# Kernel optimization log

Measured on AMD Instinct MI355X. Metric: run time of the kernel, lower is better.

Reference implementation:

```python
import jax, jax.numpy as jnp
import numpy as np

B, K, N, M = 32, 128, 128, 256  # batch, num_classes(==n_dim), n_dim, samples-per-matrix
EPSILON = 0.1
LAMBDA_SOFTMAX = 0.1
LEARNING_RATE = 0.01
BN_EPS = 1e-5


def setup_inputs() -> dict:
    key = jax.random.key(0)
    k1, k2, k3 = jax.random.split(key, 3)
    x = jax.random.normal(k1, (B, N, M), dtype=jnp.float32)
    A = jax.random.normal(k2, (K, N, N), dtype=jnp.float32) * 0.1
    EC_proto = jnp.einsum('kij,klj->kil', A, A)  # per-class PSD prototype covariances (K,N,N)
    EC_count = jax.random.uniform(k3, (K,), dtype=jnp.float32, minval=1.0, maxval=100.0)
    return {"x": x, "EC_proto": EC_proto, "EC_count": EC_count}


def reference(x, EC_proto, EC_count):
    n = x.shape[1]
    dtype = x.dtype
    # BatchNorm1d(num_classes, affine=False, track_running_stats=False): batch stats over (N, L)
    mean = x.mean(axis=(0, 2), keepdims=True)
    var = x.var(axis=(0, 2), keepdims=True)  # biased variance, as torch uses for normalization
    x = (x - mean) / jnp.sqrt(var + BN_EPS)

    eye = jnp.eye(n, dtype=dtype)
    total = EC_count.sum()
    has_counts = total > 1e-6

    # E branch: global expansion operator
    e_alpha = jnp.where(has_counts, n / (EPSILON * EPSILON * total), jnp.zeros((), dtype))
    e = e_alpha * jnp.linalg.inv(e_alpha * EC_proto.sum(0) + eye)  # (N,N)
    e_x_z = jnp.einsum('ij,bjm->bim', e, x)  # (B,N,M)

    # C branch: per-class compression operators
    bool_depth = (EC_count != 0).astype(dtype)  # (K,)
    count_fix = EC_count + (1.0 - bool_depth)
    c_alpha = (n / (count_fix * EPSILON * EPSILON) * bool_depth)[:, None, None]  # (K,1,1)
    c = c_alpha * jnp.linalg.inv(c_alpha * EC_proto + eye[None])  # (K,N,N)
    c_x_z = jnp.einsum('kij,bjm->bkim', c, x)  # (B,K,N,M)

    # Frobenius norm per (b,k), rescaled to sum to 10 over classes
    norm = jnp.sqrt((c_x_z * c_x_z).sum(axis=(2, 3)))  # (B,K)
    norm = 10.0 * norm / norm.sum(axis=1, keepdims=True)

    pi = jax.nn.softmax(-LAMBDA_SOFTMAX * norm, axis=1) * bool_depth  # (B,K)
    gama = jnp.where(has_counts, EC_count / total, jnp.zeros_like(EC_count))  # (K,)

    z_d = e_x_z - jnp.einsum('k,bkim,bk->bim', gama, c_x_z, pi)  # (B,N,M)
    return x + LEARNING_RATE * z_d
```

## Files before the change

### kernel.cpp

```cpp
#include <hip/hip_runtime.h>
#include <math.h>

#define Bb 32
#define Kk 128
#define Nn 128
#define Mm 256
#define EPS2 0.01f
#define LAMBDA_S 0.1f
#define LR 0.01f
#define BN_EPS_C 1e-5f

#define SWZ(c) (((c) & 14) | (((c) & 1) << 4) | (((c) >> 4) & 1))

__global__ void kA_bn_psum(const float* __restrict__ x, const float* __restrict__ P,
                           float* __restrict__ xn, float* __restrict__ Psum) {
  int t = threadIdx.x;
  if (blockIdx.x < 128) {
    int n = blockIdx.x;
    float s = 0.f, s2 = 0.f;
    #pragma unroll 4
    for (int b = 0; b < Bb; ++b) {
      float v = x[(size_t)b * (Nn * Mm) + n * Mm + t];
      s += v;
      s2 += v * v;
    }
    #pragma unroll
    for (int o = 32; o > 0; o >>= 1) {
      s += __shfl_down(s, o, 64);
      s2 += __shfl_down(s2, o, 64);
    }
    __shared__ float rs[4], rs2[4];
    if ((t & 63) == 0) { rs[t >> 6] = s; rs2[t >> 6] = s2; }
    __syncthreads();
    float S = rs[0] + rs[1] + rs[2] + rs[3];
    float S2 = rs2[0] + rs2[1] + rs2[2] + rs2[3];
    float mean = S * (1.0f / (Bb * Mm));
    float var = S2 * (1.0f / (Bb * Mm)) - mean * mean;
    float rstd = 1.0f / sqrtf(var + BN_EPS_C);
    #pragma unroll 4
    for (int b = 0; b < Bb; ++b) {
      size_t idx = (size_t)b * (Nn * Mm) + n * Mm + t;
      xn[idx] = (x[idx] - mean) * rstd;
    }
  } else {
    int e = (blockIdx.x - 128) * 256 + t;
    float s = 0.f;
    #pragma unroll 8
    for (int k = 0; k < Kk; ++k) s += P[(size_t)k * 16384 + e];
    Psum[e] = s;
  }
}

__global__ __launch_bounds__(256, 1) void k3S(
    const float* __restrict__ P, const float* __restrict__ Psum,
    const float* __restrict__ cnt, float* __restrict__ C,
    const float* __restrict__ xn, float* __restrict__ S) {
  __shared__ __align__(16) float LB[8448];
  int bx = blockIdx.x;
  int t = threadIdx.x;

  if (bx < 129) {
    float* Mt = LB;
    float* Rb = LB + 2112;
    float* redc = LB + 4160;
    int blk = bx;
    int tx = t & 15, ty = t >> 4;

    float cv = cnt[t & 127];
    float sr = cv;
    #pragma unroll
    for (int o = 32; o > 0; o >>= 1) sr += __shfl_down(sr, o, 64);
    if ((t & 63) == 0) redc[t >> 6] = sr;
    __syncthreads();
    float total = redc[0] + redc[1];
    bool has = total > 1e-6f;
    float av;
    if (blk < 128) {
      float c = cnt[blk];
      float bk = (c != 0.0f) ? 1.0f : 0.0f;
      float cfix = c + (1.0f - bk);
      av = (float)Nn / (cfix * EPS2) * bk;
    } else {
      av = has ? ((float)Nn / (EPS2 * total)) : 0.0f;
    }
    const float* src = (blk < 128) ? (P + (size_t)blk * 16384) : Psum;

    float a[8][8];
    #pragma unroll
    for (int i = 0; i < 8; ++i) {
      int row = ty * 8 + i;
      float4 p0 = *(const float4*)&src[row * 128 + tx * 8];
      float4 p1 = *(const float4*)&src[row * 128 + tx * 8 + 4];
      a[i][0] = av * p0.x; a[i][1] = av * p0.y; a[i][2] = av * p0.z; a[i][3] = av * p0.w;
      a[i][4] = av * p1.x; a[i][5] = av * p1.y; a[i][6] = av * p1.z; a[i][7] = av * p1.w;
      if (tx == ty) a[i][i] += 1.0f;
    }

    for (int kb = 0; kb < 8; ++kb) {
      int k0 = kb * 16;
      if ((ty >> 1) == kb) {
        int d = ty & 1;
        #pragma unroll
        for (int i = 0; i < 8; ++i) {
          *(float4*)&Rb[(d * 8 + i) * 128 + SWZ(2 * tx) * 4] =
              make_float4(a[i][0], a[i][1], a[i][2], a[i][3]);
          *(float4*)&Rb[(d * 8 + i) * 128 + SWZ(2 * tx + 1) * 4] =
              make_float4(a[i][4], a[i][5], a[i][6], a[i][7]);
        }
      }
      if ((tx >> 1) == kb) {
        int dh = tx & 1;
        #pragma unroll
        for (int i = 0; i < 8; ++i)
          #pragma unroll
          for (int j = 0; j < 8; ++j)
            Mt[(dh * 8 + j) * 132 + ty * 8 + i] = a[i][j];
      }
      __syncthreads();

      if (t < 64) {
        int l = t;
        float m[2][16];
        #pragma unroll
        for (int d = 0; d < 2; ++d)
          #pragma unroll
          for (int j = 0; j < 16; ++j)
            m[d][j] = Mt[j * 132 + 2 * l + d];
        #pragma unroll
        for (int q = 0; q < 16; ++q) {
          int lq = (k0 + q) >> 1;
          float pr[16];
          #pragma unroll
          for (int j = 0; j < 16; ++j) pr[j] = __shfl(m[q & 1][j], lq, 64);
          float pinv = 1.0f / pr[q];
          #pragma unroll
          for (int d = 0; d < 2; ++d) {
            float f = m[d][q];
            bool isp = (2 * l + d == k0 + q);
            float g = isp ? (1.0f - pinv) : f * pinv;
            #pragma unroll
            for (int j = 0; j < 16; ++j) m[d][j] = fmaf(-g, pr[j], m[d][j]);
            m[d][q] = isp ? pinv : -g;
          }
        }
        #pragma unroll
        for (int d = 0; d < 2; ++d)
          #pragma unroll
          for (int j = 0; j < 16; ++j)
            Mt[j * 132 + 2 * l + d] = m[d][j];
      }
      __syncthreads();

      if ((ty >> 1) == kb) {
        #pragma unroll
        for (int i = 0; i < 8; ++i)
          #pragma unroll
          for (int j = 0; j < 8; ++j) a[i][j] = 0.0f;
      }
      #pragma unroll
      for (int q = 0; q < 16; ++q) {
        float4 m0 = *(const float4*)&Mt[q * 132 + ty * 8];
        float4 m1 = *(const float4*)&Mt[q * 132 + ty * 8 + 4];
        float4 r0 = *(const float4*)&Rb[q * 128 + SWZ(2 * tx) * 4];
        float4 r1 = *(const float4*)&Rb[q * 128 + SWZ(2 * tx + 1) * 4];
        float mq[8] = {m0.x, m0.y, m0.z, m0.w, m1.x, m1.y, m1.z, m1.w};
        float rq[8] = {r0.x, r0.y, r0.z, r0.w, r1.x, r1.y, r1.z, r1.w};
        #pragma unroll
        for (int i = 0; i < 8; ++i)
          #pragma unroll
          for (int j = 0; j < 8; ++j)
            a[i][j] = fmaf(mq[i], rq[j], a[i][j]);
      }
      if ((tx >> 1) == kb) {
        int dh = tx & 1;
        #pragma unroll
        for (int j = 0; j < 8; ++j) {
          float4 v0 = *(const float4*)&Mt[(dh * 8 + j) * 132 + ty * 8];
          float4 v1 = *(const float4*)&Mt[(dh * 8 + j) * 132 + ty * 8 + 4];
          a[0][j] = v0.x; a[1][j] = v0.y; a[2][j] = v0.z; a[3][j] = v0.w;
          a[4][j] = v1.x; a[5][j] = v1.y; a[6][j] = v1.z; a[7][j] = v1.w;
        }
      }
      __syncthreads();
    }

    float* dst = C + (size_t)blk * 16384;
    #pragma unroll
    for (int i = 0; i < 8; ++i) {
      int row = ty * 8 + i;
      float4 v0 = make_float4(av * a[i][0], av * a[i][1], av * a[i][2], av * a[i][3]);
      float4 v1 = make_float4(av * a[i][4], av * a[i][5], av * a[i][6], av * a[i][7]);
      *(float4*)&dst[row * 128 + tx * 8] = v0;
      *(float4*)&dst[row * 128 + tx * 8 + 4] = v1;
    }
  } else {
    int bxx = bx - 129;
    int b = bxx >> 1;
    int jbase = (bxx & 1) * 64;
    float* X = LB;
    int tx = t & 15, ty = t >> 4;
    float acc[8][4] = {};
    for (int mc = 0; mc < Mm; mc += 64) {
      __syncthreads();
      for (int c = 0; c < 32; ++c) {
        int e = c * 256 + t;
        int i = e >> 6, mm = e & 63;
        X[i * 65 + mm] = xn[(size_t)b * (Nn * Mm) + i * Mm + mc + mm];
      }
      __syncthreads();
      for (int mm = 0; mm < 64; ++mm) {
        float ai[8], bj[4];
        #pragma unroll
        for (int q = 0; q < 8; ++q) ai[q] = X[(ty * 8 + q) * 65 + mm];
        #pragma unroll
        for (int q = 0; q < 4; ++q) bj[q] = X[(jbase + tx * 4 + q) * 65 + mm];
        #pragma unroll
        for (int qi = 0; qi < 8; ++qi)
          #pragma unroll
          for (int qj = 0; qj < 4; ++qj)
            acc[qi][qj] = fmaf(ai[qi], bj[qj], acc[qi][qj]);
      }
    }
    float* dst = S + (size_t)b * 16384;
    #pragma unroll
    for (int qi = 0; qi < 8; ++qi) {
      float4 v = make_float4(acc[qi][0], acc[qi][1], acc[qi][2], acc[qi][3]);
      *(float4*)&dst[(ty * 8 + qi) * 128 + jbase + tx * 4] = v;
    }
  }
}

__global__ __launch_bounds__(256, 1) void gram_k(const float* __restrict__ C,
                                                 float* __restrict__ G) {
  __shared__ __align__(16) float LB[128 * 128];
  int k = blockIdx.x >> 1, half = blockIdx.x & 1;
  int t = threadIdx.x;
  const float* src = C + (size_t)k * 16384;
  for (int c = 0; c < 64; ++c) LB[c * 256 + t] = src[c * 256 + t];
  __syncthreads();
  int tx = t & 31, ty = t >> 5;
  int i0 = half * 64 + ty * 8, j0 = tx * 4;
  float acc[8][4] = {};
  for (int l = 0; l < 128; ++l) {
    float ai[8], bj[4];
    *(float4*)&ai[0] = *(const float4*)&LB[l * 128 + i0];
    *(float4*)&ai[4] = *(const float4*)&LB[l * 128 + i0 + 4];
    *(float4*)&bj[0] = *(const float4*)&LB[l * 128 + j0];
    #pragma unroll
    for (int qi = 0; qi < 8; ++qi)
      #pragma unroll
      for (int qj = 0; qj < 4; ++qj)
        acc[qi][qj] = fmaf(ai[qi], bj[qj], acc[qi][qj]);
  }
  float* dst = G + (size_t)k * 16384;
  #pragma unroll
  for (int qi = 0; qi < 8; ++qi)
    *(float4*)&dst[(i0 + qi) * 128 + j0] =
        make_float4(acc[qi][0], acc[qi][1], acc[qi][2], acc[qi][3]);
}

__global__ __launch_bounds__(256, 1) void k6_k(const float* __restrict__ G,
                                               const float* __restrict__ S,
                                               float* __restrict__ part) {
  __shared__ __align__(16) float Gp[128 * 68];
  __shared__ __align__(16) float Sp[32 * 68];
  int c = blockIdx.x;
  int t = threadIdx.x;
  int off = c * 64;
  #pragma unroll
  for (int q = 0; q < 8; ++q) {
    int e = q * 256 + t;
    int k = e >> 4, j4 = e & 15;
    *(float4*)&Gp[k * 68 + j4 * 4] = *(const float4*)&G[(size_t)k * 16384 + off + j4 * 4];
  }
  #pragma unroll
  for (int q = 0; q < 2; ++q) {
    int e = q * 256 + t;
    int b = e >> 4, j4 = e & 15;
    *(float4*)&Sp[b * 68 + j4 * 4] = *(const float4*)&S[(size_t)b * 16384 + off + j4 * 4];
  }
  __syncthreads();
  int tk = t & 15, tb = t >> 4;
  float acc[2][8] = {};
  for (int j4 = 0; j4 < 16; ++j4) {
    float4 sv0 = *(const float4*)&Sp[(tb * 2) * 68 + j4 * 4];
    float4 sv1 = *(const float4*)&Sp[(tb * 2 + 1) * 68 + j4 * 4];
    float4 gv[8];
    #pragma unroll
    for (int q = 0; q < 8; ++q) gv[q] = *(const float4*)&Gp[(tk + 16 * q) * 68 + j4 * 4];
    #pragma unroll
    for (int q = 0; q < 8; ++q) {
      acc[0][q] = fmaf(sv0.x, gv[q].x, acc[0][q]);
      acc[0][q] = fmaf(sv0.y, gv[q].y, acc[0][q]);
      acc[0][q] = fmaf(sv0.z, gv[q].z, acc[0][q]);
      acc[0][q] = fmaf(sv0.w, gv[q].w, acc[0][q]);
      acc[1][q] = fmaf(sv1.x, gv[q].x, acc[1][q]);
      acc[1][q] = fmaf(sv1.y, gv[q].y, acc[1][q]);
      acc[1][q] = fmaf(sv1.z, gv[q].z, acc[1][q]);
      acc[1][q] = fmaf(sv1.w, gv[q].w, acc[1][q]);
    }
  }
  float* pout = part + (size_t)c * 4096;
  #pragma unroll
  for (int bb = 0; bb < 2; ++bb)
    #pragma unroll
    for (int q = 0; q < 8; ++q)
      pout[(tb * 2 + bb) * 128 + tk + 16 * q] = acc[bb][q];
}

__global__ void k7_k(const float* __restrict__ part,
                     const float* __restrict__ cnt, float* __restrict__ wT) {
  int b = blockIdx.x;
  int t = threadIdx.x;
  int k = t & 127, h = t >> 7;
  float s = 0.f;
  #pragma unroll 8
  for (int c = h * 128; c < h * 128 + 128; ++c)
    s += part[(size_t)c * 4096 + b * 128 + k];
  __shared__ float sh[256];
  sh[t] = s;
  __syncthreads();
  float norm2 = sh[k] + sh[k + 128];
  float norm = sqrtf(fmaxf(norm2, 0.0f));
  float cv = cnt[k];
  float tt = cv;
  #pragma unroll
  for (int o = 32; o > 0; o >>= 1) tt += __shfl_down(tt, o, 64);
  __shared__ float redt[4];
  if ((t & 63) == 0) redt[t >> 6] = tt;
  float r = norm;
  #pragma unroll
  for (int o = 32; o > 0; o >>= 1) r += __shfl_down(r, o, 64);
  __shared__ float red[4];
  if ((t & 63) == 0) red[t >> 6] = r;
  __syncthreads();
  float total = redt[0] + redt[1];
  float sumn = 0.5f * (red[0] + red[1] + red[2] + red[3]);
  float nr = 10.0f * norm / fmaxf(sumn, 1e-30f);
  float ex = expf(-LAMBDA_S * nr);
  float r2 = ex;
  #pragma unroll
  for (int o = 32; o > 0; o >>= 1) r2 += __shfl_down(r2, o, 64);
  __shared__ float red2[4];
  if ((t & 63) == 0) red2[t >> 6] = r2;
  __syncthreads();
  float sume = 0.5f * (red2[0] + red2[1] + red2[2] + red2[3]);
  float bk = (cv != 0.0f) ? 1.0f : 0.0f;
  float pi = (ex / sume) * bk;
  float gama = (total > 1e-6f) ? (cv / total) : 0.0f;
  if (h == 0) wT[k * 32 + b] = gama * pi;
}

__global__ __launch_bounds__(256, 1) void k8_k(const float* __restrict__ C,
                                               const float* __restrict__ E,
                                               const float* __restrict__ wT,
                                               float* __restrict__ F) {
  int e = blockIdx.x * 256 + threadIdx.x;
  int b0 = blockIdx.y * 8;
  float acc[8];
  float ev = E[e];
  #pragma unroll
  for (int b = 0; b < 8; ++b) acc[b] = ev;
  for (int k = 0; k < 128; ++k) {
    float cv = C[(size_t)k * 16384 + e];
    const float* wk = wT + k * 32 + b0;
    #pragma unroll
    for (int b = 0; b < 8; ++b) acc[b] = fmaf(-wk[b], cv, acc[b]);
  }
  #pragma unroll
  for (int b = 0; b < 8; ++b) F[(size_t)(b0 + b) * 16384 + e] = acc[b];
}

__global__ __launch_bounds__(256, 1) void k9_k(const float* __restrict__ F,
                                               const float* __restrict__ xn,
                                               float* __restrict__ out) {
  int bx = blockIdx.x;
  int b = bx >> 3, y = bx & 7;
  int mq = y >> 1, ih = y & 1;
  __shared__ __align__(16) float Ft[64 * 68];
  __shared__ __align__(16) float Xt[64 * 68];
  int t = threadIdx.x;
  int tx = t & 15, ty = t >> 4;
  float acc[4][4] = {};
  for (int jc = 0; jc < 128; jc += 64) {
    __syncthreads();
    #pragma unroll
    for (int q = 0; q < 4; ++q) {
      int e = q * 256 + t;
      int i = e >> 4, j4 = e & 15;
      *(float4*)&Ft[i * 68 + j4 * 4] =
          *(const float4*)&F[(size_t)b * 16384 + (ih * 64 + i) * 128 + jc + j4 * 4];
    }
    #pragma unroll
    for (int q = 0; q < 4; ++q) {
      int e = q * 256 + t;
      int jj = e >> 4, m4 = e & 15;
      *(float4*)&Xt[jj * 68 + m4 * 4] =
          *(const float4*)&xn[(size_t)b * (Nn * Mm) + (jc + jj) * Mm + mq * 64 + m4 * 4];
    }
    __syncthreads();
    for (int j4 = 0; j4 < 16; ++j4) {
      float4 fi[4], xm[4];
      #pragma unroll
      for (int r = 0; r < 4; ++r)
        fi[r] = *(const float4*)&Ft[(ty * 4 + r) * 68 + j4 * 4];
      #pragma unroll
      for (int r = 0; r < 4; ++r)
        xm[r] = *(const float4*)&Xt[(j4 * 4 + r) * 68 + tx * 4];
      #pragma unroll
      for (int qi = 0; qi < 4; ++qi) {
        #pragma unroll
        for (int qm = 0; qm < 4; ++qm) {
          float xv = ((const float*)&xm[0])[qm];
          acc[qi][qm] = fmaf(fi[qi].x, xv, acc[qi][qm]);
          xv = ((const float*)&xm[1])[qm];
          acc[qi][qm] = fmaf(fi[qi].y, xv, acc[qi][qm]);
          xv = ((const float*)&xm[2])[qm];
          acc[qi][qm] = fmaf(fi[qi].z, xv, acc[qi][qm]);
          xv = ((const float*)&xm[3])[qm];
          acc[qi][qm] = fmaf(fi[qi].w, xv, acc[qi][qm]);
        }
      }
    }
  }
  int i0 = ih * 64 + ty * 4, m0 = mq * 64 + tx * 4;
  #pragma unroll
  for (int qi = 0; qi < 4; ++qi) {
    float4 xv = *(const float4*)&xn[(size_t)b * (Nn * Mm) + (i0 + qi) * Mm + m0];
    float4 o;
    o.x = fmaf(LR, acc[qi][0], xv.x);
    o.y = fmaf(LR, acc[qi][1], xv.y);
    o.z = fmaf(LR, acc[qi][2], xv.z);
    o.w = fmaf(LR, acc[qi][3], xv.w);
    *(float4*)&out[(size_t)b * (Nn * Mm) + (i0 + qi) * Mm + m0] = o;
  }
}

extern "C" void kernel_launch(void* const* d_in, const int* in_sizes, int n_in,
                              void* d_out, int out_size, void* d_ws, size_t ws_size,
                              hipStream_t stream) {
  const float* x = (const float*)d_in[0];
  const float* P = (const float*)d_in[1];
  const float* cnt = (const float*)d_in[2];
  float* out = (float*)d_out;

  float* ws = (float*)d_ws;
  float* xn = ws;
  float* C = xn + 1048576;
  float* G = C + 2113536;
  float* S = G + 2097152;
  float* part = S + 524288;
  float* F = part + 1048576;
  float* wT = F + 524288;
  float* Psum = wT + 4096;
  size_t need_bytes = (size_t)((Psum + 16384) - ws) * sizeof(float);
  if (ws_size < need_bytes) return;

  hipLaunchKernelGGL(kA_bn_psum, dim3(192), dim3(256), 0, stream, x, P, xn, Psum);
  hipLaunchKernelGGL(k3S, dim3(193), dim3(256), 0, stream, P, Psum, cnt, C, xn, S);
  hipLaunchKernelGGL(gram_k, dim3(256), dim3(256), 0, stream, C, G);
  hipLaunchKernelGGL(k6_k, dim3(256), dim3(256), 0, stream, G, S, part);
  hipLaunchKernelGGL(k7_k, dim3(32), dim3(256), 0, stream, part, cnt, wT);
  hipLaunchKernelGGL(k8_k, dim3(64, 4), dim3(256), 0, stream, C,
                     C + (size_t)128 * 16384, wT, F);
  hipLaunchKernelGGL(k9_k, dim3(256), dim3(256), 0, stream, F, xn, out);
}
```

Before: 177.5 us.

## Fuse Gram-norm contraction and softmax-weighted apply into two kernels

Merges the Gram computation with the per-batch norm contraction so the Gram matrices stay in shared memory and are reduced directly against S, never written to global memory. Also merges the softmax weighting, the weighted sum of compression operators and the final apply GEMM into one kernel that keeps F in shared memory. This cuts five launches to two and removes the large global round-trips for G, part and F. The cost is that the softmax is recomputed serially by eight threads per block, and the apply kernel has only 128 blocks and reads xn straight from global memory without tiling, which may leave the GPU underused.

```diff
diff --git a/kernel.cpp b/kernel.cpp
--- a/kernel.cpp
+++ b/kernel.cpp
@@ -230,16 +230,18 @@
   }
 }
 
-__global__ __launch_bounds__(256, 1) void gram_k(const float* __restrict__ C,
-                                                 float* __restrict__ G) {
+__global__ __launch_bounds__(256, 1) void kGN(const float* __restrict__ C,
+                                              const float* __restrict__ S,
+                                              float* __restrict__ norm2h) {
   __shared__ __align__(16) float LB[128 * 128];
-  int k = blockIdx.x >> 1, half = blockIdx.x & 1;
+  __shared__ float redb[4][32];
+  int k = blockIdx.x >> 1, h = blockIdx.x & 1;
   int t = threadIdx.x;
   const float* src = C + (size_t)k * 16384;
   for (int c = 0; c < 64; ++c) LB[c * 256 + t] = src[c * 256 + t];
   __syncthreads();
-  int tx = t & 31, ty = t >> 5;
-  int i0 = half * 64 + ty * 8, j0 = tx * 4;
+  int tx = t & 15, ty = t >> 4;
+  int i0 = ty * 8, j0 = h * 64 + tx * 4;
   float acc[8][4] = {};
   for (int l = 0; l < 128; ++l) {
     float ai[8], bj[4];
@@ -252,187 +254,159 @@
       for (int qj = 0; qj < 4; ++qj)
         acc[qi][qj] = fmaf(ai[qi], bj[qj], acc[qi][qj]);
   }
-  float* dst = G + (size_t)k * 16384;
+  __syncthreads();
   #pragma unroll
   for (int qi = 0; qi < 8; ++qi)
-    *(float4*)&dst[(i0 + qi) * 128 + j0] =
+    *(float4*)&LB[(i0 + qi) * 64 + tx * 4] =
         make_float4(acc[qi][0], acc[qi][1], acc[qi][2], acc[qi][3]);
-}
-
-__global__ __launch_bounds__(256, 1) void k6_k(const float* __restrict__ G,
-                                               const float* __restrict__ S,
-                                               float* __restrict__ part) {
-  __shared__ __align__(16) float Gp[128 * 68];
-  __shared__ __align__(16) float Sp[32 * 68];
-  int c = blockIdx.x;
-  int t = threadIdx.x;
-  int off = c * 64;
+  __syncthreads();
+  float nacc[32];
+  #pragma unroll
+  for (int b = 0; b < 32; ++b) nacc[b] = 0.0f;
   #pragma unroll
   for (int q = 0; q < 8; ++q) {
-    int e = q * 256 + t;
-    int k = e >> 4, j4 = e & 15;
-    *(float4*)&Gp[k * 68 + j4 * 4] = *(const float4*)&G[(size_t)k * 16384 + off + j4 * 4];
+    int el = (q * 256 + t) * 4;
+    float4 g = *(const float4*)&LB[el];
+    int i = el >> 6, jl = el & 63;
+    const float* sb = S + i * 128 + h * 64 + jl;
+    #pragma unroll
+    for (int b = 0; b < 32; ++b) {
+      float4 sv = *(const float4*)&sb[(size_t)b * 16384];
+      nacc[b] = fmaf(g.x, sv.x, nacc[b]);
+      nacc[b] = fmaf(g.y, sv.y, nacc[b]);
+      nacc[b] = fmaf(g.z, sv.z, nacc[b]);
+      nacc[b] = fmaf(g.w, sv.w, nacc[b]);
+    }
   }
   #pragma unroll
-  for (int q = 0; q < 2; ++q) {
-    int e = q * 256 + t;
-    int b = e >> 4, j4 = e & 15;
-    *(float4*)&Sp[b * 68 + j4 * 4] = *(const float4*)&S[(size_t)b * 16384 + off + j4 * 4];
-  }
-  __syncthreads();
-  int tk = t & 15, tb = t >> 4;
-  float acc[2][8] = {};
-  for (int j4 = 0; j4 < 16; ++j4) {
-    float4 sv0 = *(const float4*)&Sp[(tb * 2) * 68 + j4 * 4];
-    float4 sv1 = *(const float4*)&Sp[(tb * 2 + 1) * 68 + j4 * 4];
-    float4 gv[8];
-    #pragma unroll
-    for (int q = 0; q < 8; ++q) gv[q] = *(const float4*)&Gp[(tk + 16 * q) * 68 + j4 * 4];
-    #pragma unroll
-    for (int q = 0; q < 8; ++q) {
-      acc[0][q] = fmaf(sv0.x, gv[q].x, acc[0][q]);
-      acc[0][q] = fmaf(sv0.y, gv[q].y, acc[0][q]);
-      acc[0][q] = fmaf(sv0.z, gv[q].z, acc[0][q]);
-      acc[0][q] = fmaf(sv0.w, gv[q].w, acc[0][q]);
-      acc[1][q] = fmaf(sv1.x, gv[q].x, acc[1][q]);
-      acc[1][q] = fmaf(sv1.y, gv[q].y, acc[1][q]);
-      acc[1][q] = fmaf(sv1.z, gv[q].z, acc[1][q]);
-      acc[1][q] = fmaf(sv1.w, gv[q].w, acc[1][q]);
-    }
-  }
-  float* pout = part + (size_t)c * 4096;
-  #pragma unroll
-  for (int bb = 0; bb < 2; ++bb)
-    #pragma unroll
-    for (int q = 0; q < 8; ++q)
-      pout[(tb * 2 + bb) * 128 + tk + 16 * q] = acc[bb][q];
+  for (int b = 0; b < 32; ++b) {
+    float v = nacc[b];
+    #pragma unroll
+    for (int o = 32; o > 0; o >>= 1) v += __shfl_down(v, o, 64);
+    nacc[b] = v;
+  }
+  if ((t & 63) == 0) {
+    int w = t >> 6;
+    #pragma unroll
+    for (int b = 0; b < 32; ++b) redb[w][b] = nacc[b];
+  }
+  __syncthreads();
+  if (t < 32)
+    norm2h[(size_t)k * 64 + h * 32 + t] =
+        redb[0][t] + redb[1][t] + redb[2][t] + redb[3][t];
 }
 
-__global__ void k7_k(const float* __restrict__ part,
-                     const float* __restrict__ cnt, float* __restrict__ wT) {
-  int b = blockIdx.x;
+__global__ __launch_bounds__(256, 1) void k89(const float* __restrict__ C,
+                                              const float* __restrict__ norm2h,
+                                              const float* __restrict__ cnt,
+                                              const float* __restrict__ xn,
+                                              float* __restrict__ out) {
+  __shared__ float wTs[128 * 8];
+  __shared__ __align__(16) float Fs[8 * 4 * 128];
+  int bx = blockIdx.x;
+  int bg = bx >> 5, ig = bx & 31;
+  int b0 = bg * 8, i0 = ig * 4;
   int t = threadIdx.x;
-  int k = t & 127, h = t >> 7;
-  float s = 0.f;
-  #pragma unroll 8
-  for (int c = h * 128; c < h * 128 + 128; ++c)
-    s += part[(size_t)c * 4096 + b * 128 + k];
-  __shared__ float sh[256];
-  sh[t] = s;
-  __syncthreads();
-  float norm2 = sh[k] + sh[k + 128];
-  float norm = sqrtf(fmaxf(norm2, 0.0f));
-  float cv = cnt[k];
-  float tt = cv;
-  #pragma unroll
-  for (int o = 32; o > 0; o >>= 1) tt += __shfl_down(tt, o, 64);
-  __shared__ float redt[4];
-  if ((t & 63) == 0) redt[t >> 6] = tt;
-  float r = norm;
-  #pragma unroll
-  for (int o = 32; o > 0; o >>= 1) r += __shfl_down(r, o, 64);
-  __shared__ float red[4];
-  if ((t & 63) == 0) red[t >> 6] = r;
-  __syncthreads();
-  float total = redt[0] + redt[1];
-  float sumn = 0.5f * (red[0] + red[1] + red[2] + red[3]);
-  float nr = 10.0f * norm / fmaxf(sumn, 1e-30f);
-  float ex = expf(-LAMBDA_S * nr);
-  float r2 = ex;
-  #pragma unroll
-  for (int o = 32; o > 0; o >>= 1) r2 += __shfl_down(r2, o, 64);
-  __shared__ float red2[4];
-  if ((t & 63) == 0) red2[t >> 6] = r2;
-  __syncthreads();
-  float sume = 0.5f * (red2[0] + red2[1] + red2[2] + red2[3]);
-  float bk = (cv != 0.0f) ? 1.0f : 0.0f;
-  float pi = (ex / sume) * bk;
-  float gama = (total > 1e-6f) ? (cv / total) : 0.0f;
-  if (h == 0) wT[k * 32 + b] = gama * pi;
-}
-
-__global__ __launch_bounds__(256, 1) void k8_k(const float* __restrict__ C,
-                                               const float* __restrict__ E,
-                                               const float* __restrict__ wT,
-                                               float* __restrict__ F) {
-  int e = blockIdx.x * 256 + threadIdx.x;
-  int b0 = blockIdx.y * 8;
-  float acc[8];
-  float ev = E[e];
-  #pragma unroll
-  for (int b = 0; b < 8; ++b) acc[b] = ev;
-  for (int k = 0; k < 128; ++k) {
-    float cv = C[(size_t)k * 16384 + e];
-    const float* wk = wT + k * 32 + b0;
-    #pragma unroll
-    for (int b = 0; b < 8; ++b) acc[b] = fmaf(-wk[b], cv, acc[b]);
-  }
-  #pragma unroll
-  for (int b = 0; b < 8; ++b) F[(size_t)(b0 + b) * 16384 + e] = acc[b];
-}
-
-__global__ __launch_bounds__(256, 1) void k9_k(const float* __restrict__ F,
-                                               const float* __restrict__ xn,
-                                               float* __restrict__ out) {
-  int bx = blockIdx.x;
-  int b = bx >> 3, y = bx & 7;
-  int mq = y >> 1, ih = y & 1;
-  __shared__ __align__(16) float Ft[64 * 68];
-  __shared__ __align__(16) float Xt[64 * 68];
-  int t = threadIdx.x;
-  int tx = t & 15, ty = t >> 4;
-  float acc[4][4] = {};
-  for (int jc = 0; jc < 128; jc += 64) {
-    __syncthreads();
-    #pragma unroll
-    for (int q = 0; q < 4; ++q) {
-      int e = q * 256 + t;
-      int i = e >> 4, j4 = e & 15;
-      *(float4*)&Ft[i * 68 + j4 * 4] =
-          *(const float4*)&F[(size_t)b * 16384 + (ih * 64 + i) * 128 + jc + j4 * 4];
-    }
-    #pragma unroll
-    for (int q = 0; q < 4; ++q) {
-      int e = q * 256 + t;
-      int jj = e >> 4, m4 = e & 15;
-      *(float4*)&Xt[jj * 68 + m4 * 4] =
-          *(const float4*)&xn[(size_t)b * (Nn * Mm) + (jc + jj) * Mm + mq * 64 + m4 * 4];
-    }
-    __syncthreads();
-    for (int j4 = 0; j4 < 16; ++j4) {
-      float4 fi[4], xm[4];
-      #pragma unroll
-      for (int r = 0; r < 4; ++r)
-        fi[r] = *(const float4*)&Ft[(ty * 4 + r) * 68 + j4 * 4];
-      #pragma unroll
-      for (int r = 0; r < 4; ++r)
-        xm[r] = *(const float4*)&Xt[(j4 * 4 + r) * 68 + tx * 4];
-      #pragma unroll
-      for (int qi = 0; qi < 4; ++qi) {
-        #pragma unroll
-        for (int qm = 0; qm < 4; ++qm) {
-          float xv = ((const float*)&xm[0])[qm];
-          acc[qi][qm] = fmaf(fi[qi].x, xv, acc[qi][qm]);
-          xv = ((const float*)&xm[1])[qm];
-          acc[qi][qm] = fmaf(fi[qi].y, xv, acc[qi][qm]);
-          xv = ((const float*)&xm[2])[qm];
-          acc[qi][qm] = fmaf(fi[qi].z, xv, acc[qi][qm]);
-          xv = ((const float*)&xm[3])[qm];
-          acc[qi][qm] = fmaf(fi[qi].w, xv, acc[qi][qm]);
+  const float* E = C + (size_t)128 * 16384;
+
+  if (t < 8) {
+    int b = b0 + t;
+    float total = 0.f;
+    for (int k = 0; k < 128; ++k) total += cnt[k];
+    bool has = total > 1e-6f;
+    float sumn = 0.f;
+    float norms[128];
+    for (int k = 0; k < 128; ++k) {
+      float n2 = norm2h[(size_t)k * 64 + b] + norm2h[(size_t)k * 64 + 32 + b];
+      float nv = sqrtf(fmaxf(n2, 0.0f));
+      norms[k] = nv;
+      sumn += nv;
+    }
+    float inv_sumn = 10.0f / fmaxf(sumn, 1e-30f);
+    float sume = 0.f;
+    for (int k = 0; k < 128; ++k) {
+      float ex = expf(-LAMBDA_S * (norms[k] * inv_sumn));
+      norms[k] = ex;
+      sume += ex;
+    }
+    float inv_sume = 1.0f / sume;
+    for (int k = 0; k < 128; ++k) {
+      float cv = cnt[k];
+      float bk = (cv != 0.0f) ? 1.0f : 0.0f;
+      float pi = norms[k] * inv_sume * bk;
+      float gama = has ? (cv / total) : 0.0f;
+      wTs[k * 8 + t] = gama * pi;
+    }
+  }
+  __syncthreads();
+
+  {
+    int j4 = (t & 31) * 4, g = t >> 5;
+    float4 acc4[4];
+    #pragma unroll
+    for (int ii = 0; ii < 4; ++ii)
+      acc4[ii] = *(const float4*)&E[(i0 + ii) * 128 + j4];
+    for (int k = 0; k < 128; ++k) {
+      float w = wTs[k * 8 + g];
+      #pragma unroll
+      for (int ii = 0; ii < 4; ++ii) {
+        float4 cv = *(const float4*)&C[(size_t)k * 16384 + (i0 + ii) * 128 + j4];
+        acc4[ii].x = fmaf(-w, cv.x, acc4[ii].x);
+        acc4[ii].y = fmaf(-w, cv.y, acc4[ii].y);
+        acc4[ii].z = fmaf(-w, cv.z, acc4[ii].z);
+        acc4[ii].w = fmaf(-w, cv.w, acc4[ii].w);
+      }
+    }
+    #pragma unroll
+    for (int ii = 0; ii < 4; ++ii)
+      *(float4*)&Fs[g * 512 + ii * 128 + j4] = acc4[ii];
+  }
+  __syncthreads();
+
+  {
+    int hw = t >> 5, lane = t & 31;
+    int b = b0 + hw, m0 = lane * 8;
+    const float* xb = xn + (size_t)b * (Nn * Mm);
+    float4 acc[4][2] = {};
+    for (int j = 0; j < 128; j += 4) {
+      float4 fr[4];
+      #pragma unroll
+      for (int ii = 0; ii < 4; ++ii)
+        fr[ii] = *(const float4*)&Fs[hw * 512 + ii * 128 + j];
+      float4 xr[4][2];
+      #pragma unroll
+      for (int jj = 0; jj < 4; ++jj) {
+        xr[jj][0] = *(const float4*)&xb[(j + jj) * Mm + m0];
+        xr[jj][1] = *(const float4*)&xb[(j + jj) * Mm + m0 + 4];
+      }
+      #pragma unroll
+      for (int ii = 0; ii < 4; ++ii) {
+        const float fv[4] = {fr[ii].x, fr[ii].y, fr[ii].z, fr[ii].w};
+        #pragma unroll
+        for (int jj = 0; jj < 4; ++jj) {
+          #pragma unroll
+          for (int half = 0; half < 2; ++half) {
+            acc[ii][half].x = fmaf(fv[jj], xr[jj][half].x, acc[ii][half].x);
+            acc[ii][half].y = fmaf(fv[jj], xr[jj][half].y, acc[ii][half].y);
+            acc[ii][half].z = fmaf(fv[jj], xr[jj][half].z, acc[ii][half].z);
+            acc[ii][half].w = fmaf(fv[jj], xr[jj][half].w, acc[ii][half].w);
+          }
         }
       }
     }
-  }
-  int i0 = ih * 64 + ty * 4, m0 = mq * 64 + tx * 4;
-  #pragma unroll
-  for (int qi = 0; qi < 4; ++qi) {
-    float4 xv = *(const float4*)&xn[(size_t)b * (Nn * Mm) + (i0 + qi) * Mm + m0];
-    float4 o;
-    o.x = fmaf(LR, acc[qi][0], xv.x);
-    o.y = fmaf(LR, acc[qi][1], xv.y);
-    o.z = fmaf(LR, acc[qi][2], xv.z);
-    o.w = fmaf(LR, acc[qi][3], xv.w);
-    *(float4*)&out[(size_t)b * (Nn * Mm) + (i0 + qi) * Mm + m0] = o;
+    #pragma unroll
+    for (int ii = 0; ii < 4; ++ii) {
+      #pragma unroll
+      for (int half = 0; half < 2; ++half) {
+        float4 xv = *(const float4*)&xb[(i0 + ii) * Mm + m0 + half * 4];
+        float4 o;
+        o.x = fmaf(LR, acc[ii][half].x, xv.x);
+        o.y = fmaf(LR, acc[ii][half].y, xv.y);
+        o.z = fmaf(LR, acc[ii][half].z, xv.z);
+        o.w = fmaf(LR, acc[ii][half].w, xv.w);
+        *(float4*)&out[(size_t)b * (Nn * Mm) + (i0 + ii) * Mm + m0 + half * 4] = o;
+      }
+    }
   }
 }
 
@@ -447,21 +421,14 @@
   float* ws = (float*)d_ws;
   float* xn = ws;
   float* C = xn + 1048576;
-  float* G = C + 2113536;
-  float* S = G + 2097152;
-  float* part = S + 524288;
-  float* F = part + 1048576;
-  float* wT = F + 524288;
-  float* Psum = wT + 4096;
+  float* S = C + 2113536;
+  float* norm2h = S + 524288;
+  float* Psum = norm2h + 8192;
   size_t need_bytes = (size_t)((Psum + 16384) - ws) * sizeof(float);
   if (ws_size < need_bytes) return;
 
   hipLaunchKernelGGL(kA_bn_psum, dim3(192), dim3(256), 0, stream, x, P, xn, Psum);
   hipLaunchKernelGGL(k3S, dim3(193), dim3(256), 0, stream, P, Psum, cnt, C, xn, S);
-  hipLaunchKernelGGL(gram_k, dim3(256), dim3(256), 0, stream, C, G);
-  hipLaunchKernelGGL(k6_k, dim3(256), dim3(256), 0, stream, G, S, part);
-  hipLaunchKernelGGL(k7_k, dim3(32), dim3(256), 0, stream, part, cnt, wT);
-  hipLaunchKernelGGL(k8_k, dim3(64, 4), dim3(256), 0, stream, C,
-                     C + (size_t)128 * 16384, wT, F);
-  hipLaunchKernelGGL(k9_k, dim3(256), dim3(256), 0, stream, F, xn, out);
+  hipLaunchKernelGGL(kGN, dim3(256), dim3(256), 0, stream, C, S, norm2h);
+  hipLaunchKernelGGL(k89, dim3(128), dim3(256), 0, stream, C, norm2h, cnt, xn, out);
 }
```

Result: slower. 216.1 us (+21.7%).

## Fuse Gram computation with norm contraction and drop the partial-sum buffer

Applied to the files above, without the earlier changes.

Merges the per-class Gram kernel with the kernel that contracts it against S, so each block keeps its half of C^T C in shared memory and reduces it directly against all 32 batch slices. This removes the round trip of the 8 MB G buffer and the large partial-sum array, and k7 becomes a 128-thread reduction over only two partials. The cost is that every block now reads S from global memory for all batches with strided float4 loads, and each thread holds 32 accumulators, which raises register pressure.

```diff
diff --git a/kernel.cpp b/kernel.cpp
--- a/kernel.cpp
+++ b/kernel.cpp
@@ -230,16 +230,18 @@
   }
 }
 
-__global__ __launch_bounds__(256, 1) void gram_k(const float* __restrict__ C,
-                                                 float* __restrict__ G) {
+__global__ __launch_bounds__(256, 1) void kGN(const float* __restrict__ C,
+                                              const float* __restrict__ S,
+                                              float* __restrict__ norm2h) {
   __shared__ __align__(16) float LB[128 * 128];
-  int k = blockIdx.x >> 1, half = blockIdx.x & 1;
+  __shared__ float redb[4][32];
+  int k = blockIdx.x >> 1, h = blockIdx.x & 1;
   int t = threadIdx.x;
   const float* src = C + (size_t)k * 16384;
   for (int c = 0; c < 64; ++c) LB[c * 256 + t] = src[c * 256 + t];
   __syncthreads();
-  int tx = t & 31, ty = t >> 5;
-  int i0 = half * 64 + ty * 8, j0 = tx * 4;
+  int tx = t & 15, ty = t >> 4;
+  int i0 = ty * 8, j0 = h * 64 + tx * 4;
   float acc[8][4] = {};
   for (int l = 0; l < 128; ++l) {
     float ai[8], bj[4];
@@ -252,103 +254,78 @@
       for (int qj = 0; qj < 4; ++qj)
         acc[qi][qj] = fmaf(ai[qi], bj[qj], acc[qi][qj]);
   }
-  float* dst = G + (size_t)k * 16384;
+  __syncthreads();
   #pragma unroll
   for (int qi = 0; qi < 8; ++qi)
-    *(float4*)&dst[(i0 + qi) * 128 + j0] =
+    *(float4*)&LB[(i0 + qi) * 64 + tx * 4] =
         make_float4(acc[qi][0], acc[qi][1], acc[qi][2], acc[qi][3]);
-}
-
-__global__ __launch_bounds__(256, 1) void k6_k(const float* __restrict__ G,
-                                               const float* __restrict__ S,
-                                               float* __restrict__ part) {
-  __shared__ __align__(16) float Gp[128 * 68];
-  __shared__ __align__(16) float Sp[32 * 68];
-  int c = blockIdx.x;
-  int t = threadIdx.x;
-  int off = c * 64;
+  __syncthreads();
+  float nacc[32];
+  #pragma unroll
+  for (int b = 0; b < 32; ++b) nacc[b] = 0.0f;
   #pragma unroll
   for (int q = 0; q < 8; ++q) {
-    int e = q * 256 + t;
-    int k = e >> 4, j4 = e & 15;
-    *(float4*)&Gp[k * 68 + j4 * 4] = *(const float4*)&G[(size_t)k * 16384 + off + j4 * 4];
-  }
-  #pragma unroll
-  for (int q = 0; q < 2; ++q) {
-    int e = q * 256 + t;
-    int b = e >> 4, j4 = e & 15;
-    *(float4*)&Sp[b * 68 + j4 * 4] = *(const float4*)&S[(size_t)b * 16384 + off + j4 * 4];
-  }
-  __syncthreads();
-  int tk = t & 15, tb = t >> 4;
-  float acc[2][8] = {};
-  for (int j4 = 0; j4 < 16; ++j4) {
-    float4 sv0 = *(const float4*)&Sp[(tb * 2) * 68 + j4 * 4];
-    float4 sv1 = *(const float4*)&Sp[(tb * 2 + 1) * 68 + j4 * 4];
-    float4 gv[8];
-    #pragma unroll
-    for (int q = 0; q < 8; ++q) gv[q] = *(const float4*)&Gp[(tk + 16 * q) * 68 + j4 * 4];
-    #pragma unroll
-    for (int q = 0; q < 8; ++q) {
-      acc[0][q] = fmaf(sv0.x, gv[q].x, acc[0][q]);
-      acc[0][q] = fmaf(sv0.y, gv[q].y, acc[0][q]);
-      acc[0][q] = fmaf(sv0.z, gv[q].z, acc[0][q]);
-      acc[0][q] = fmaf(sv0.w, gv[q].w, acc[0][q]);
-      acc[1][q] = fmaf(sv1.x, gv[q].x, acc[1][q]);
-      acc[1][q] = fmaf(sv1.y, gv[q].y, acc[1][q]);
-      acc[1][q] = fmaf(sv1.z, gv[q].z, acc[1][q]);
-      acc[1][q] = fmaf(sv1.w, gv[q].w, acc[1][q]);
-    }
-  }
-  float* pout = part + (size_t)c * 4096;
-  #pragma unroll
-  for (int bb = 0; bb < 2; ++bb)
-    #pragma unroll
-    for (int q = 0; q < 8; ++q)
-      pout[(tb * 2 + bb) * 128 + tk + 16 * q] = acc[bb][q];
-}
-
-__global__ void k7_k(const float* __restrict__ part,
-                     const float* __restrict__ cnt, float* __restrict__ wT) {
+    int el = (q * 256 + t) * 4;
+    float4 g = *(const float4*)&LB[el];
+    int i = el >> 6, jl = el & 63;
+    const float* sb = S + i * 128 + h * 64 + jl;
+    #pragma unroll
+    for (int b = 0; b < 32; ++b) {
+      float4 sv = *(const float4*)&sb[(size_t)b * 16384];
+      nacc[b] = fmaf(g.x, sv.x, nacc[b]);
+      nacc[b] = fmaf(g.y, sv.y, nacc[b]);
+      nacc[b] = fmaf(g.z, sv.z, nacc[b]);
+      nacc[b] = fmaf(g.w, sv.w, nacc[b]);
+    }
+  }
+  #pragma unroll
+  for (int b = 0; b < 32; ++b) {
+    float v = nacc[b];
+    #pragma unroll
+    for (int o = 32; o > 0; o >>= 1) v += __shfl_down(v, o, 64);
+    nacc[b] = v;
+  }
+  if ((t & 63) == 0) {
+    int w = t >> 6;
+    #pragma unroll
+    for (int b = 0; b < 32; ++b) redb[w][b] = nacc[b];
+  }
+  __syncthreads();
+  if (t < 32)
+    norm2h[(size_t)k * 64 + h * 32 + t] =
+        redb[0][t] + redb[1][t] + redb[2][t] + redb[3][t];
+}
+
+__global__ void k7n(const float* __restrict__ norm2h, const float* __restrict__ cnt,
+                    float* __restrict__ wT) {
   int b = blockIdx.x;
-  int t = threadIdx.x;
-  int k = t & 127, h = t >> 7;
-  float s = 0.f;
-  #pragma unroll 8
-  for (int c = h * 128; c < h * 128 + 128; ++c)
-    s += part[(size_t)c * 4096 + b * 128 + k];
-  __shared__ float sh[256];
-  sh[t] = s;
-  __syncthreads();
-  float norm2 = sh[k] + sh[k + 128];
-  float norm = sqrtf(fmaxf(norm2, 0.0f));
+  int k = threadIdx.x;
+  float n2 = norm2h[(size_t)k * 64 + b] + norm2h[(size_t)k * 64 + 32 + b];
+  float norm = sqrtf(fmaxf(n2, 0.0f));
   float cv = cnt[k];
-  float tt = cv;
-  #pragma unroll
-  for (int o = 32; o > 0; o >>= 1) tt += __shfl_down(tt, o, 64);
-  __shared__ float redt[4];
-  if ((t & 63) == 0) redt[t >> 6] = tt;
-  float r = norm;
-  #pragma unroll
-  for (int o = 32; o > 0; o >>= 1) r += __shfl_down(r, o, 64);
-  __shared__ float red[4];
-  if ((t & 63) == 0) red[t >> 6] = r;
-  __syncthreads();
-  float total = redt[0] + redt[1];
-  float sumn = 0.5f * (red[0] + red[1] + red[2] + red[3]);
+  __shared__ float r1[2], r2[2], r3[2];
+  float tt = cv, r = norm;
+  #pragma unroll
+  for (int o = 32; o > 0; o >>= 1) {
+    tt += __shfl_down(tt, o, 64);
+    r += __shfl_down(r, o, 64);
+  }
+  if ((k & 63) == 0) { r1[k >> 6] = tt; r2[k >> 6] = r; }
+  __syncthreads();
+  float total = r1[0] + r1[1];
+  float sumn = r2[0] + r2[1];
   float nr = 10.0f * norm / fmaxf(sumn, 1e-30f);
   float ex = expf(-LAMBDA_S * nr);
-  float r2 = ex;
-  #pragma unroll
-  for (int o = 32; o > 0; o >>= 1) r2 += __shfl_down(r2, o, 64);
-  __shared__ float red2[4];
-  if ((t & 63) == 0) red2[t >> 6] = r2;
-  __syncthreads();
-  float sume = 0.5f * (red2[0] + red2[1] + red2[2] + red2[3]);
+  float e2 = ex;
+  #pragma unroll
+  for (int o = 32; o > 0; o >>= 1) e2 += __shfl_down(e2, o, 64);
+  if ((k & 63) == 0) r3[k >> 6] = e2;
+  __syncthreads();
+  float sume = r3[0] + r3[1];
   float bk = (cv != 0.0f) ? 1.0f : 0.0f;
   float pi = (ex / sume) * bk;
   float gama = (total > 1e-6f) ? (cv / total) : 0.0f;
-  if (h == 0) wT[k * 32 + b] = gama * pi;
+  wT[k * 32 + b] = gama * pi;
 }
 
 __global__ __launch_bounds__(256, 1) void k8_k(const float* __restrict__ C,
@@ -447,20 +424,18 @@
   float* ws = (float*)d_ws;
   float* xn = ws;
   float* C = xn + 1048576;
-  float* G = C + 2113536;
-  float* S = G + 2097152;
-  float* part = S + 524288;
-  float* F = part + 1048576;
-  float* wT = F + 524288;
-  float* Psum = wT + 4096;
+  float* S = C + 2113536;
+  float* norm2h = S + 524288;
+  float* wT = norm2h + 8192;
+  float* F = wT + 4096;
+  float* Psum = F + 524288;
   size_t need_bytes = (size_t)((Psum + 16384) - ws) * sizeof(float);
   if (ws_size < need_bytes) return;
 
   hipLaunchKernelGGL(kA_bn_psum, dim3(192), dim3(256), 0, stream, x, P, xn, Psum);
   hipLaunchKernelGGL(k3S, dim3(193), dim3(256), 0, stream, P, Psum, cnt, C, xn, S);
-  hipLaunchKernelGGL(gram_k, dim3(256), dim3(256), 0, stream, C, G);
-  hipLaunchKernelGGL(k6_k, dim3(256), dim3(256), 0, stream, G, S, part);
-  hipLaunchKernelGGL(k7_k, dim3(32), dim3(256), 0, stream, part, cnt, wT);
+  hipLaunchKernelGGL(kGN, dim3(256), dim3(256), 0, stream, C, S, norm2h);
+  hipLaunchKernelGGL(k7n, dim3(32), dim3(128), 0, stream, norm2h, cnt, wT);
   hipLaunchKernelGGL(k8_k, dim3(64, 4), dim3(256), 0, stream, C,
                      C + (size_t)128 * 16384, wT, F);
   hipLaunchKernelGGL(k9_k, dim3(256), dim3(256), 0, stream, F, xn, out);
```

New measurement: 169.3 us. 1.05x faster.
